# Optimization experiments

Measured on AMD Instinct MI355X. Metric: run time of the kernel, lower is better.

The kernel has to match this reference:

```python
import jax, jax.numpy as jnp
import numpy as np

INV_SQRT2 = 0.7071067811865476
BETA = 0.3
LN_EPS = 1e-5

B, S, P, C, TD = 128, 1024, 336, 128, 4
H1, H2, K = C // 4, C // 8, 3  # rda=4, rdb=8, ksize=3


def setup_inputs() -> dict:
    key = jax.random.key(0)
    ks = jax.random.split(key, 20)
    rn = lambda k, sh: jax.random.normal(k, sh, dtype=jnp.float32)
    return {
        "x": rn(ks[0], (B, S, C)),
        "x_mark_enc": rn(ks[1], (B, S, TD)),
        "x_dec": rn(ks[2], (B, P, C)),
        "y_mark_dec": rn(ks[3], (B, P, TD)),
        # time_enc params
        "W1": rn(ks[4], (H1, TD)) * 0.1, "b1": jnp.zeros((H1,), jnp.float32),
        "g1": jnp.ones((H1,), jnp.float32), "be1": jnp.zeros((H1,), jnp.float32),
        "W2": rn(ks[5], (H2, H1)) * 0.1, "b2": jnp.zeros((H2,), jnp.float32),
        "g2": jnp.ones((H2,), jnp.float32), "be2": jnp.zeros((H2,), jnp.float32),
        "Wc": rn(ks[6], (S, S, K)) * 0.02, "bc": jnp.zeros((S,), jnp.float32),
        "W3": rn(ks[7], (C, H2)) * 0.1, "b3": jnp.zeros((C,), jnp.float32),
        # projections
        "Wtp": rn(ks[8], (P, S)) * 0.02, "btp": jnp.zeros((P,), jnp.float32),
        "Whp": rn(ks[9], (P, S)) * 0.02, "bhp": jnp.zeros((P,), jnp.float32),
    }


def _haar_level1(x):
    # pywt.wavedec(sig, 'db1', level=1) -> [cA, cD]; concat along time.
    # For even length: cA[k]=(x[2k]+x[2k+1])/sqrt(2), cD[k]=(x[2k]-x[2k+1])/sqrt(2).
    xe, xo = x[:, 0::2, :], x[:, 1::2, :]
    cA = (xe + xo) * INV_SQRT2
    cD = (xe - xo) * INV_SQRT2
    return jnp.concatenate([cA, cD], axis=1)  # [B, S, C]


def _layernorm(h, g, b):
    m = jnp.mean(h, axis=-1, keepdims=True)
    v = jnp.mean((h - m) ** 2, axis=-1, keepdims=True)
    return (h - m) * jax.lax.rsqrt(v + LN_EPS) * g + b


def reference(x, x_mark_enc, x_dec, y_mark_dec,
              W1, b1, g1, be1, W2, b2, g2, be2, Wc, bc, W3, b3,
              Wtp, btp, Whp, bhp):
    # wavelet transform + instance norm over time (torch.var is unbiased)
    xw = _haar_level1(x)
    means = jnp.mean(xw, axis=1, keepdims=True)
    stdev = jnp.sqrt(jnp.var(xw, axis=1, ddof=1, keepdims=True) + 1e-5)
    xn = (xw - means) / stdev

    # time_enc MLP: Linear -> LN -> ReLU -> Linear -> LN -> ReLU
    h = jax.nn.relu(_layernorm(jnp.einsum('bst,ht->bsh', x_mark_enc, W1) + b1, g1, be1))
    h = jax.nn.relu(_layernorm(jnp.einsum('bsh,gh->bsg', h, W2) + b2, g2, be2))
    # Conv1d(in=seq_len, out=seq_len, k=3, padding='same') over feature dim H2
    h = jax.lax.conv_general_dilated(h, Wc, window_strides=(1,), padding='SAME',
                                     dimension_numbers=('NCH', 'OIH', 'NCH'))
    h = h + bc[None, :, None]
    time_embed = jnp.einsum('bsg,cg->bsc', h, W3) + b3  # [B, S, C]

    # seq->pred projections (Linear over time axis), then blend
    time_out = jnp.einsum('bsc,ps->bpc', time_embed, Wtp) + btp[None, :, None]
    pred = jnp.einsum('bsc,ps->bpc', xn, Whp) + bhp[None, :, None]
    pred = BETA * pred + (1.0 - BETA) * time_out
    pred = pred * stdev + means
    return pred  # [B, P, C] == dec_out[:, -pred_len:, :]
```

## Files before the change

kernel.cpp:

```cpp
#include <hip/hip_runtime.h>
#include <hip/hip_bf16.h>

#define INV_SQRT2f 0.70710678118654752440f
#define BETAf 0.3f
#define OMBf  0.7f
#define LN_EPSf 1e-5f

#define B 128
#define S 1024
#define P 336
#define C 128
#define H1 32
#define H2 16

#define WS_WHP2G  0
#define WS_EPI    262144
#define WS_BCP    296448
#define WS_H2     296832
#define WS_WCPT   2393984
#define WS_M      2393984
#define WS_AIMG   3426176

typedef short  s16x8 __attribute__((ext_vector_type(8)));
typedef float  f32x4 __attribute__((ext_vector_type(4)));

__device__ __forceinline__ unsigned f2bf(float f) {
    unsigned u = __float_as_uint(f);
    return (u + 0x7fffu + ((u >> 16) & 1u)) >> 16;
}

__device__ __forceinline__ int whp2l_u32(int p, int sp) {
    int kt   = sp >> 4;
    int tile = kt * 2 + p / 192;
    int sub  = (p % 192) >> 4;
    int kg   = (sp & 15) >> 2;
    int m    = p & 15;
    int byte = tile * 12288 + sub * 1024 + kg * 256 + m * 16 + 4 * (sp & 3);
    return byte >> 2;
}

__global__ void k_prep(const float* __restrict__ Whp, const float* __restrict__ Wtp,
                       const float* __restrict__ bc,  const float* __restrict__ bhp,
                       const float* __restrict__ btp, float* __restrict__ ws)
{
    const int p = blockIdx.x;
    const int t = threadIdx.x;
    unsigned* img = (unsigned*)ws;
    __shared__ float red[768];
    float sw = 0.f, rw = 0.f, bp = 0.f;
    for (int sp = t; sp < 512; sp += 256) {
        float a = Whp[p * 1024 + sp];
        float d = Whp[p * 1024 + 512 + sp];
        float va = BETAf * (a + d) * INV_SQRT2f;
        float vb = BETAf * (a - d) * INV_SQRT2f;
        img[whp2l_u32(p, sp)] = f2bf(va) | (f2bf(vb) << 16);
        sw += a + d;
    }
    for (int s = t; s < S; s += 256) {
        float w = Wtp[p * 1024 + s];
        rw += w;
        bp += w * bc[s];
    }
    red[t] = sw; red[256 + t] = rw; red[512 + t] = bp;
    __syncthreads();
    for (int off = 128; off > 0; off >>= 1) {
        if (t < off) {
            red[t]       += red[t + off];
            red[256 + t] += red[256 + t + off];
            red[512 + t] += red[512 + t + off];
        }
        __syncthreads();
    }
    if (t == 0) {
        ws[WS_BCP + p] = red[512];
        float* e = ws + WS_EPI + p * 4;
        e[0] = BETAf * bhp[p] + OMBf * btp[p];
        e[1] = OMBf * red[256];
        e[2] = 1.f - BETAf * red[0];
        e[3] = 0.f;
    }
}

__global__ void k_mlp(const float* __restrict__ xme,
                      const float* __restrict__ W1, const float* __restrict__ b1,
                      const float* __restrict__ g1, const float* __restrict__ be1,
                      const float* __restrict__ W2, const float* __restrict__ b2,
                      const float* __restrict__ g2, const float* __restrict__ be2,
                      float* __restrict__ ws)
{
    __shared__ float w1s[128], b1s[32], g1s[32], be1s[32];
    __shared__ float w2s[512], b2s[16], g2s[16], be2s[16];
    const int t = threadIdx.x;
    if (t < 128) w1s[t] = W1[t];
    if (t < 32) { b1s[t] = b1[t]; g1s[t] = g1[t]; be1s[t] = be1[t]; }
    for (int i = t; i < 512; i += 256) w2s[i] = W2[i];
    if (t < 16) { b2s[t] = b2[t]; g2s[t] = g2[t]; be2s[t] = be2[t]; }
    __syncthreads();

    const int row = blockIdx.x * 256 + t;
    float4 v = *(const float4*)(xme + (size_t)row * 4);

    float h1v[32];
    float m = 0.f;
    #pragma unroll
    for (int i = 0; i < 32; i++) {
        float a = w1s[i*4+0]*v.x + w1s[i*4+1]*v.y + w1s[i*4+2]*v.z + w1s[i*4+3]*v.w + b1s[i];
        h1v[i] = a; m += a;
    }
    m *= (1.f / 32.f);
    float var = 0.f;
    #pragma unroll
    for (int i = 0; i < 32; i++) { float d = h1v[i] - m; var += d * d; }
    var *= (1.f / 32.f);
    float rs = rsqrtf(var + LN_EPSf);
    #pragma unroll
    for (int i = 0; i < 32; i++)
        h1v[i] = fmaxf((h1v[i] - m) * rs * g1s[i] + be1s[i], 0.f);

    float h2v[16];
    float m2 = 0.f;
    #pragma unroll
    for (int g = 0; g < 16; g++) {
        float a = b2s[g];
        #pragma unroll
        for (int i = 0; i < 32; i++) a = fmaf(w2s[g * 32 + i], h1v[i], a);
        h2v[g] = a; m2 += a;
    }
    m2 *= (1.f / 16.f);
    float v2 = 0.f;
    #pragma unroll
    for (int g = 0; g < 16; g++) { float d = h2v[g] - m2; v2 += d * d; }
    v2 *= (1.f / 16.f);
    float rs2 = rsqrtf(v2 + LN_EPSf);
    float* h2o = ws + WS_H2 + (size_t)row * 16;
    #pragma unroll
    for (int g = 0; g < 16; g++)
        h2o[g] = fmaxf((h2v[g] - m2) * rs2 * g2s[g] + be2s[g], 0.f);
}

__global__ __launch_bounds__(256) void k_wcp(const float* __restrict__ Wc,
                                             const float* __restrict__ Wtp,
                                             float* __restrict__ ws)
{
    __shared__ __align__(16) unsigned short Bs[2][4][4][16][8];
    const int pbase = blockIdx.x * 96;
    const int n0    = blockIdx.y * 64;
    const int t     = threadIdx.x;
    const int lane  = t & 63;
    const int wid   = t >> 6;
    const int wm    = wid >> 1;
    const int wn    = wid & 1;
    const int g8    = lane >> 4;
    const int n16   = lane & 15;

    const int bn  = t & 63;
    const int bkg = t >> 6;

    int prow[3];
    #pragma unroll
    for (int fi = 0; fi < 3; fi++) {
        int pr = pbase + wm * 48 + fi * 16 + n16;
        prow[fi] = pr < P ? pr : P - 1;
    }

#define LOADB_(dst, kt) {                                                   \
    const float* xs_ = Wc + (size_t)((kt) * 32 + 8 * bkg) * 3072 + n0 + bn; \
    _Pragma("unroll")                                                       \
    for (int e_ = 0; e_ < 8; e_++) dst[e_] = xs_[(size_t)e_ * 3072]; }

#define WRITEB_(src, buf) {                                                 \
    uint4 w_;                                                               \
    w_.x = f2bf(src[0]) | (f2bf(src[1]) << 16);                             \
    w_.y = f2bf(src[2]) | (f2bf(src[3]) << 16);                             \
    w_.z = f2bf(src[4]) | (f2bf(src[5]) << 16);                             \
    w_.w = f2bf(src[6]) | (f2bf(src[7]) << 16);                             \
    *(uint4*)&Bs[buf][bn >> 4][bkg][bn & 15][0] = w_; }

#define LOADA_(dst, kt) {                                                   \
    _Pragma("unroll")                                                       \
    for (int fi_ = 0; fi_ < 3; fi_++) {                                     \
        const float* as_ = Wtp + (size_t)prow[fi_] * 1024 + (kt) * 32 + g8 * 8; \
        dst[fi_][0] = *(const float4*)(as_);                                \
        dst[fi_][1] = *(const float4*)(as_ + 4); } }

#define PACKA_(fa, src) {                                                   \
    _Pragma("unroll")                                                       \
    for (int fi_ = 0; fi_ < 3; fi_++) {                                     \
        uint4 w_;                                                           \
        w_.x = f2bf(src[fi_][0].x) | (f2bf(src[fi_][0].y) << 16);           \
        w_.y = f2bf(src[fi_][0].z) | (f2bf(src[fi_][0].w) << 16);           \
        w_.z = f2bf(src[fi_][1].x) | (f2bf(src[fi_][1].y) << 16);           \
        w_.w = f2bf(src[fi_][1].z) | (f2bf(src[fi_][1].w) << 16);           \
        fa[fi_] = *(s16x8*)&w_; } }

#define MFMA6_(buf, fa) {                                                   \
    s16x8 fb0 = *(const s16x8*)&Bs[buf][2 * wn + 0][g8][n16][0];            \
    s16x8 fb1 = *(const s16x8*)&Bs[buf][2 * wn + 1][g8][n16][0];            \
    _Pragma("unroll")                                                       \
    for (int fi_ = 0; fi_ < 3; fi_++) {                                     \
        acc[fi_][0] = __builtin_amdgcn_mfma_f32_16x16x32_bf16(fa[fi_], fb0, acc[fi_][0], 0, 0, 0); \
        acc[fi_][1] = __builtin_amdgcn_mfma_f32_16x16x32_bf16(fa[fi_], fb1, acc[fi_][1], 0, 0, 0); } }

    f32x4 acc[3][2];
    #pragma unroll
    for (int i = 0; i < 3; i++) {
        acc[i][0] = (f32x4){0.f, 0.f, 0.f, 0.f};
        acc[i][1] = (f32x4){0.f, 0.f, 0.f, 0.f};
    }

    float  b0r[8], b1r[8];
    float4 a0r[3][2], a1r[3][2];

    LOADA_(a0r, 0); LOADB_(b0r, 0);
    LOADA_(a1r, 1); LOADB_(b1r, 1);
    WRITEB_(b0r, 0);
    __syncthreads();

    for (int i = 0; i < 16; i++) {
        const int kt = 2 * i;
        {
            s16x8 fa[3];
            PACKA_(fa, a0r);
            if (kt + 2 < 32) { LOADA_(a0r, kt + 2); LOADB_(b0r, kt + 2); }
            MFMA6_(0, fa);
        }
        __syncthreads();
        WRITEB_(b1r, 1);
        __syncthreads();
        {
            s16x8 fa[3];
            PACKA_(fa, a1r);
            if (kt + 3 < 32) { LOADA_(a1r, kt + 3); LOADB_(b1r, kt + 3); }
            MFMA6_(1, fa);
        }
        __syncthreads();
        if (kt + 2 < 32) WRITEB_(b0r, 0);
        __syncthreads();
    }

#undef LOADB_
#undef WRITEB_
#undef LOADA_
#undef PACKA_
#undef MFMA6_

    float* wcT = ws + WS_WCPT;
    #pragma unroll
    for (int fi = 0; fi < 3; fi++) {
        #pragma unroll
        for (int r = 0; r < 4; r++) {
            int p = pbase + wm * 48 + fi * 16 + g8 * 4 + r;
            if (p < P) {
                wcT[(size_t)p * 3072 + n0 + wn * 32 + 0 * 16 + n16] = acc[fi][0][r];
                wcT[(size_t)p * 3072 + n0 + wn * 32 + 1 * 16 + n16] = acc[fi][1][r];
            }
        }
    }
}

__global__ void k_repack(float* __restrict__ ws)
{
    const int l  = threadIdx.x;
    const int ch = blockIdx.x;
    const int pf = blockIdx.y;
    const int k  = ch >> 5;
    const int i0 = (ch & 31) * 32 + (l >> 4) * 8;
    const int p  = pf * 16 + (l & 15);
    uint4 w = make_uint4(0, 0, 0, 0);
    if (p < P) {
        const float* wcT = ws + WS_WCPT + (size_t)p * 3072;
        float v[8];
        #pragma unroll
        for (int e = 0; e < 8; e++)
            v[e] = wcT[(i0 + e) * 3 + k];
        w.x = f2bf(v[0]) | (f2bf(v[1]) << 16);
        w.y = f2bf(v[2]) | (f2bf(v[3]) << 16);
        w.z = f2bf(v[4]) | (f2bf(v[5]) << 16);
        w.w = f2bf(v[6]) | (f2bf(v[7]) << 16);
    }
    ((uint4*)(ws + WS_AIMG))[(size_t)(ch * 24 + pf) * 64 + l] = w;
}

#define HT_RS 1056
__global__ __launch_bounds__(256) void k_mconv(float* __restrict__ ws)
{
    __shared__ unsigned short Ht[18 * HT_RS];
    const int b  = blockIdx.x;
    const int pt = blockIdx.y;
    const int t  = threadIdx.x;
    const int l  = t & 63;
    const int wid = t >> 6;
    const int pf = pt * 4 + wid;
    const int n16 = l & 15;
    const int g8  = l >> 4;

    for (int j = t; j < HT_RS; j += 256) {
        Ht[j] = 0;
        Ht[17 * HT_RS + j] = 0;
    }
    {
        const float* h2b = ws + WS_H2 + (size_t)b * 16384;
        const int s0 = t * 4;
        float v[4][16];
        #pragma unroll
        for (int rr = 0; rr < 4; rr++) {
            const float4* src = (const float4*)(h2b + (size_t)(s0 + rr) * 16);
            float4 a0 = src[0], a1 = src[1], a2 = src[2], a3 = src[3];
            v[rr][0]=a0.x; v[rr][1]=a0.y; v[rr][2]=a0.z; v[rr][3]=a0.w;
            v[rr][4]=a1.x; v[rr][5]=a1.y; v[rr][6]=a1.z; v[rr][7]=a1.w;
            v[rr][8]=a2.x; v[rr][9]=a2.y; v[rr][10]=a2.z; v[rr][11]=a2.w;
            v[rr][12]=a3.x; v[rr][13]=a3.y; v[rr][14]=a3.z; v[rr][15]=a3.w;
        }
        #pragma unroll
        for (int g = 0; g < 16; g++) {
            uint2 w;
            w.x = f2bf(v[0][g]) | (f2bf(v[1][g]) << 16);
            w.y = f2bf(v[2][g]) | (f2bf(v[3][g]) << 16);
            *(uint2*)&Ht[(g + 1) * HT_RS + s0] = w;
        }
    }
    __syncthreads();

    const uint4* ap = (const uint4*)(ws + WS_AIMG) + (size_t)pf * 64 + l;
    f32x4 acc = (f32x4){0.f, 0.f, 0.f, 0.f};
    uint4 fan = *ap;
    #pragma unroll 4
    for (int it = 0; it < 96; it++) {
        uint4 fac = fan;
        ap += 24 * 64;
        if (it < 95) fan = *ap;
        const int k  = it >> 5;
        const int kt = it & 31;
        s16x8 fb = *(const s16x8*)&Ht[(n16 + k) * HT_RS + kt * 32 + g8 * 8];
        s16x8 fa = *(s16x8*)&fac;
        acc = __builtin_amdgcn_mfma_f32_16x16x32_bf16(fa, fb, acc, 0, 0, 0);
    }

    #pragma unroll
    for (int r = 0; r < 4; r++) {
        int p = pf * 16 + g8 * 4 + r;
        if (p < P)
            ws[WS_M + ((size_t)b * P + p) * 16 + n16] = acc[r] + ws[WS_BCP + p];
    }
}

__global__ __launch_bounds__(512, 1) void k_pred(
    const float* __restrict__ x,
    const float* __restrict__ W3, const float* __restrict__ b3,
    const float* __restrict__ ws, float* __restrict__ out)
{
    __shared__ __align__(16) unsigned short Bs[2][8][4][16][8];
    __shared__ float sev[512], ssq[512], smean[128], sstd[128];
    const int b     = blockIdx.x;
    const int ptile = blockIdx.y;
    const int t     = threadIdx.x;
    const int lane  = t & 63;
    const int wid   = t >> 6;
    const int wm    = wid >> 1;
    const int wn    = wid & 1;
    const int g8    = lane >> 4;
    const int n16   = lane & 15;

    const int sc  = t & 127;
    const int skg = t >> 7;

    const float* xb = x + (size_t)b * S * C;
    const char* aimgc = (const char*)ws + ptile * 12288
        + (wm * 3) * 1024 + g8 * 256 + n16 * 16;

    f32x4 acc[3][4];
    #pragma unroll
    for (int i = 0; i < 3; i++)
        #pragma unroll
        for (int j = 0; j < 4; j++) acc[i][j] = (f32x4){0.f, 0.f, 0.f, 0.f};

    float ev_acc = 0.f, sq_acc = 0.f;

#define P_LOADB_(dst, kt) {                                                 \
    const float* xs_ = xb + (size_t)(32 * (kt) + 8 * skg) * C + sc;         \
    _Pragma("unroll")                                                       \
    for (int e_ = 0; e_ < 8; e_++) dst[e_] = xs_[(size_t)e_ * C]; }

#define P_WRITEB_(src, buf) {                                               \
    uint4 w_;                                                               \
    w_.x = f2bf(src[0]) | (f2bf(src[1]) << 16);                             \
    w_.y = f2bf(src[2]) | (f2bf(src[3]) << 16);                             \
    w_.z = f2bf(src[4]) | (f2bf(src[5]) << 16);                             \
    w_.w = f2bf(src[6]) | (f2bf(src[7]) << 16);                             \
    *(uint4*)&Bs[buf][sc >> 4][skg][sc & 15][0] = w_;                       \
    _Pragma("unroll")                                                       \
    for (int e_ = 0; e_ < 8; e_++) {                                        \
        float v_ = src[e_];                                                 \
        sq_acc = fmaf(v_, v_, sq_acc);                                      \
        if ((e_ & 1) == 0) ev_acc += v_;    \
    } }

#define P_LOADA_(dst, kt) {                                                 \
    const char* ap_ = aimgc + (size_t)(kt) * 24576;                         \
    _Pragma("unroll")                                                       \
    for (int fi_ = 0; fi_ < 3; fi_++)                                       \
        dst[fi_] = *(const uint4*)(ap_ + fi_ * 1024); }

#define P_MFMA_(buf, au) {                                                  \
    s16x8 fb0 = *(const s16x8*)&Bs[buf][4 * wn + 0][g8][n16][0];            \
    s16x8 fb1 = *(const s16x8*)&Bs[buf][4 * wn + 1][g8][n16][0];            \
    s16x8 fb2 = *(const s16x8*)&Bs[buf][4 * wn + 2][g8][n16][0];            \
    s16x8 fb3 = *(const s16x8*)&Bs[buf][4 * wn + 3][g8][n16][0];            \
    _Pragma("unroll")                                                       \
    for (int fi_ = 0; fi_ < 3; fi_++) {                                     \
        s16x8 fa_ = *(s16x8*)&au[fi_];                                      \
        acc[fi_][0] = __builtin_amdgcn_mfma_f32_16x16x32_bf16(fa_, fb0, acc[fi_][0], 0, 0, 0); \
        acc[fi_][1] = __builtin_amdgcn_mfma_f32_16x16x32_bf16(fa_, fb1, acc[fi_][1], 0, 0, 0); \
        acc[fi_][2] = __builtin_amdgcn_mfma_f32_16x16x32_bf16(fa_, fb2, acc[fi_][2], 0, 0, 0); \
        acc[fi_][3] = __builtin_amdgcn_mfma_f32_16x16x32_bf16(fa_, fb3, acc[fi_][3], 0, 0, 0); } }

    float b0r[8], b1r[8];
    uint4 a0u[3], a1u[3];

    P_LOADB_(b0r, 0); P_LOADB_(b1r, 1);
    P_LOADA_(a0u, 0); P_LOADA_(a1u, 1);
    P_WRITEB_(b0r, 0);
    __syncthreads();

    for (int i = 0; i < 16; i++) {
        const int kt = 2 * i;
        {
            uint4 au[3];
            #pragma unroll
            for (int fi = 0; fi < 3; fi++) au[fi] = a0u[fi];
            if (kt + 2 < 32) { P_LOADA_(a0u, kt + 2); P_LOADB_(b0r, kt + 2); }
            P_MFMA_(0, au);
            P_WRITEB_(b1r, 1);
            __syncthreads();
        }
        {
            const int kt1 = kt + 1;
            uint4 au[3];
            #pragma unroll
            for (int fi = 0; fi < 3; fi++) au[fi] = a1u[fi];
            if (kt1 + 2 < 32) { P_LOADA_(a1u, kt1 + 2); P_LOADB_(b1r, kt1 + 2); }
            P_MFMA_(1, au);
            if (kt1 < 31) P_WRITEB_(b0r, 0);
            __syncthreads();
        }
    }

#undef P_LOADB_
#undef P_WRITEB_
#undef P_LOADA_
#undef P_MFMA_

    sev[t] = ev_acc; ssq[t] = sq_acc;
    __syncthreads();
    if (t < 128) {
        float ev = sev[t] + sev[t + 128] + sev[t + 256] + sev[t + 384];
        float sq = ssq[t] + ssq[t + 128] + ssq[t + 256] + ssq[t + 384];
        float mean = ev * (INV_SQRT2f / 512.f);
        float var  = (sq - 1024.f * mean * mean) * (1.f / 1023.f);
        smean[t] = mean;
        sstd[t]  = sqrtf(var + LN_EPSf);
    }
    __syncthreads();

    const int cb = wn * 64 + n16;
    float sdv[4], mnv[4], b3v[4];
    f32x4 w3r[4][4];
    #pragma unroll
    for (int fj = 0; fj < 4; fj++) {
        int c = cb + fj * 16;
        sdv[fj] = sstd[c];
        mnv[fj] = smean[c];
        b3v[fj] = b3[c];
        const f32x4* wr = (const f32x4*)(W3 + c * 16);
        #pragma unroll
        for (int q = 0; q < 4; q++) w3r[fj][q] = wr[q];
    }
    const int prow0 = ptile * 192 + wm * 48 + g8 * 4;
    #pragma unroll
    for (int fi = 0; fi < 3; fi++) {
        #pragma unroll
        for (int r = 0; r < 4; r++) {
            int p  = prow0 + fi * 16 + r;
            int pc = p < P ? p : P - 1;
            const f32x4* mrow = (const f32x4*)(ws + WS_M + ((size_t)b * P + pc) * 16);
            f32x4 m0 = mrow[0], m1 = mrow[1], m2 = mrow[2], m3 = mrow[3];
            const float* e = ws + WS_EPI + pc * 4;
            float A13 = e[0], A4 = e[1], A2 = e[2];
            #pragma unroll
            for (int fj = 0; fj < 4; fj++) {
                float s = 0.f;
                #pragma unroll
                for (int q = 0; q < 4; q++) {
                    const f32x4 mv = (q==0)?m0:(q==1)?m1:(q==2)?m2:m3;
                    s = fmaf(mv.x, w3r[fj][q].x, s);
                    s = fmaf(mv.y, w3r[fj][q].y, s);
                    s = fmaf(mv.z, w3r[fj][q].z, s);
                    s = fmaf(mv.w, w3r[fj][q].w, s);
                }
                float res = acc[fi][fj][r]
                          + sdv[fj] * (OMBf * s + A13 + A4 * b3v[fj])
                          + A2 * mnv[fj];
                if (p < P)
                    out[((size_t)b * P + p) * C + cb + fj * 16] = res;
            }
        }
    }
}

extern "C" void kernel_launch(void* const* d_in, const int* in_sizes, int n_in,
                              void* d_out, int out_size, void* d_ws, size_t ws_size,
                              hipStream_t stream)
{
    const float* x    = (const float*)d_in[0];
    const float* xme  = (const float*)d_in[1];
    const float* W1   = (const float*)d_in[4];
    const float* b1   = (const float*)d_in[5];
    const float* g1   = (const float*)d_in[6];
    const float* be1  = (const float*)d_in[7];
    const float* W2   = (const float*)d_in[8];
    const float* b2   = (const float*)d_in[9];
    const float* g2   = (const float*)d_in[10];
    const float* be2  = (const float*)d_in[11];
    const float* Wc   = (const float*)d_in[12];
    const float* bc   = (const float*)d_in[13];
    const float* W3   = (const float*)d_in[14];
    const float* b3   = (const float*)d_in[15];
    const float* Wtp  = (const float*)d_in[16];
    const float* btp  = (const float*)d_in[17];
    const float* Whp  = (const float*)d_in[18];
    const float* bhp  = (const float*)d_in[19];
    float* ws  = (float*)d_ws;
    float* out = (float*)d_out;

    k_prep  <<<dim3(P),      dim3(256), 0, stream>>>(Whp, Wtp, bc, bhp, btp, ws);
    k_mlp   <<<dim3(512),    dim3(256), 0, stream>>>(xme, W1, b1, g1, be1,
                                                     W2, b2, g2, be2, ws);
    k_wcp   <<<dim3(4, 48),  dim3(256), 0, stream>>>(Wc, Wtp, ws);
    k_repack<<<dim3(96, 24), dim3(64),  0, stream>>>(ws);
    k_mconv <<<dim3(B, 6),   dim3(256), 0, stream>>>(ws);
    k_pred  <<<dim3(B, 2),   dim3(512), 0, stream>>>(x, W3, b3, ws, out);
}
```

Baseline: 104.7 us.

## Fuse bf16 repack into k_wcp epilogue and deepen A-fragment prefetch in k_mconv

The k_wcp epilogue now converts its accumulators to bf16 and scatters them straight into the MFMA A-fragment image, so the separate k_repack kernel and its fp32 intermediate buffer are gone. This removes one launch and a full fp32 write plus strided re-read of the Wtp·Wc product. k_mconv also prefetches four A fragments per group instead of one, giving more loads in flight. The trade-off is scattered 2-byte global stores in the k_wcp epilogue, which may coalesce poorly.

```diff
diff --git a/kernel.cpp b/kernel.cpp
--- a/kernel.cpp
+++ b/kernel.cpp
@@ -17,7 +17,6 @@
 #define WS_EPI    262144
 #define WS_BCP    296448
 #define WS_H2     296832
-#define WS_WCPT   2393984
 #define WS_M      2393984
 #define WS_AIMG   3426176
 
@@ -244,41 +243,28 @@
 #undef PACKA_
 #undef MFMA6_
 
-    float* wcT = ws + WS_WCPT;
+    unsigned short* aimg16 = (unsigned short*)(ws + WS_AIMG);
     #pragma unroll
     for (int fi = 0; fi < 3; fi++) {
         #pragma unroll
-        for (int r = 0; r < 4; r++) {
-            int p = pbase + wm * 48 + fi * 16 + g8 * 4 + r;
-            if (p < P) {
-                wcT[(size_t)p * 3072 + n0 + wn * 32 + 0 * 16 + n16] = acc[fi][0][r];
-                wcT[(size_t)p * 3072 + n0 + wn * 32 + 1 * 16 + n16] = acc[fi][1][r];
+        for (int q = 0; q < 2; q++) {
+            const int m3 = n0 + wn * 32 + q * 16 + n16;
+            const int iq = m3 / 3;
+            const int k  = m3 - 3 * iq;
+            const int ch = k * 32 + (iq >> 5);
+            const int lh = ((iq >> 3) & 3) << 4;
+            const int e  = iq & 7;
+            #pragma unroll
+            for (int r = 0; r < 4; r++) {
+                const int p  = pbase + wm * 48 + fi * 16 + g8 * 4 + r;
+                const int pf = p >> 4;
+                const int l  = lh | (p & 15);
+                unsigned short v = (p < P) ? (unsigned short)f2bf(acc[fi][q][r])
+                                           : (unsigned short)0;
+                aimg16[((size_t)(ch * 24 + pf) * 64 + l) * 8 + e] = v;
             }
         }
     }
-}
-
-__global__ void k_repack(float* __restrict__ ws)
-{
-    const int l  = threadIdx.x;
-    const int ch = blockIdx.x;
-    const int pf = blockIdx.y;
-    const int k  = ch >> 5;
-    const int i0 = (ch & 31) * 32 + (l >> 4) * 8;
-    const int p  = pf * 16 + (l & 15);
-    uint4 w = make_uint4(0, 0, 0, 0);
-    if (p < P) {
-        const float* wcT = ws + WS_WCPT + (size_t)p * 3072;
-        float v[8];
-        #pragma unroll
-        for (int e = 0; e < 8; e++)
-            v[e] = wcT[(i0 + e) * 3 + k];
-        w.x = f2bf(v[0]) | (f2bf(v[1]) << 16);
-        w.y = f2bf(v[2]) | (f2bf(v[3]) << 16);
-        w.z = f2bf(v[4]) | (f2bf(v[5]) << 16);
-        w.w = f2bf(v[6]) | (f2bf(v[7]) << 16);
-    }
-    ((uint4*)(ws + WS_AIMG))[(size_t)(ch * 24 + pf) * 64 + l] = w;
 }
 
 #define HT_RS 1056
@@ -321,19 +307,34 @@
     }
     __syncthreads();
 
-    const uint4* ap = (const uint4*)(ws + WS_AIMG) + (size_t)pf * 64 + l;
+    const uint4* ab = (const uint4*)(ws + WS_AIMG);
+    const size_t lidx = (size_t)pf * 64 + l;
     f32x4 acc = (f32x4){0.f, 0.f, 0.f, 0.f};
-    uint4 fan = *ap;
-    #pragma unroll 4
-    for (int it = 0; it < 96; it++) {
-        uint4 fac = fan;
-        ap += 24 * 64;
-        if (it < 95) fan = *ap;
-        const int k  = it >> 5;
-        const int kt = it & 31;
-        s16x8 fb = *(const s16x8*)&Ht[(n16 + k) * HT_RS + kt * 32 + g8 * 8];
-        s16x8 fa = *(s16x8*)&fac;
-        acc = __builtin_amdgcn_mfma_f32_16x16x32_bf16(fa, fb, acc, 0, 0, 0);
+
+    uint4 nf0 = ab[lidx + (size_t)0 * 1536];
+    uint4 nf1 = ab[lidx + (size_t)1 * 1536];
+    uint4 nf2 = ab[lidx + (size_t)2 * 1536];
+    uint4 nf3 = ab[lidx + (size_t)3 * 1536];
+
+    for (int g = 0; g < 24; g++) {
+        uint4 c0 = nf0, c1 = nf1, c2 = nf2, c3 = nf3;
+        if (g < 23) {
+            const size_t nb = lidx + (size_t)(g + 1) * 4 * 1536;
+            nf0 = ab[nb];
+            nf1 = ab[nb + 1536];
+            nf2 = ab[nb + 2 * 1536];
+            nf3 = ab[nb + 3 * 1536];
+        }
+        #pragma unroll
+        for (int e = 0; e < 4; e++) {
+            const int it = 4 * g + e;
+            const int k  = it >> 5;
+            const int kt = it & 31;
+            s16x8 fb = *(const s16x8*)&Ht[(n16 + k) * HT_RS + kt * 32 + g8 * 8];
+            uint4 ce = (e == 0) ? c0 : (e == 1) ? c1 : (e == 2) ? c2 : c3;
+            s16x8 fa = *(s16x8*)&ce;
+            acc = __builtin_amdgcn_mfma_f32_16x16x32_bf16(fa, fb, acc, 0, 0, 0);
+        }
     }
 
     #pragma unroll
@@ -536,7 +537,6 @@
     k_mlp   <<<dim3(512),    dim3(256), 0, stream>>>(xme, W1, b1, g1, be1,
                                                      W2, b2, g2, be2, ws);
     k_wcp   <<<dim3(4, 48),  dim3(256), 0, stream>>>(Wc, Wtp, ws);
-    k_repack<<<dim3(96, 24), dim3(64),  0, stream>>>(ws);
     k_mconv <<<dim3(B, 6),   dim3(256), 0, stream>>>(ws);
     k_pred  <<<dim3(B, 2),   dim3(512), 0, stream>>>(x, W3, b3, ws, out);
 }
```

New measurement: 98.10 us. -6.3%, faster.
